# Optimization experiments

Measured on AMD Instinct MI355X. Metric: run time of the kernel, lower is better.

The kernel has to match this reference:

```python
import jax, jax.numpy as jnp
import numpy as np

B, N, D, H = 4, 4096, 256, 8
HD = D // H
EPS = 1e-09


def _feature_map(t):
    # ELU(x) + 1, strictly positive feature map (Katharopoulos et al. 2020)
    return jax.nn.elu(t) + 1.0


def setup_inputs() -> dict:
    key = jax.random.key(0)
    ks = jax.random.split(key, 8)
    s = 0.02  # weight init scale for numerical stability
    return {
        "x": jax.random.normal(ks[0], (B, N, D), dtype=jnp.float32),
        "prior": jax.random.normal(ks[1], (B, N, N), dtype=jnp.float32),
        "Wq": jax.random.normal(ks[2], (D, D), dtype=jnp.float32) * s,
        "Wk": jax.random.normal(ks[3], (D, D), dtype=jnp.float32) * s,
        "Wv": jax.random.normal(ks[4], (D, D), dtype=jnp.float32) * s,
        "bv": jax.random.normal(ks[5], (D,), dtype=jnp.float32) * s,
        "Wo": jax.random.normal(ks[6], (D, D), dtype=jnp.float32) * s,
        "bo": jax.random.normal(ks[7], (D,), dtype=jnp.float32) * s,
    }


def reference(x, prior, Wq, Wk, Wv, bv, Wo, bo):
    b, n, d = x.shape
    # bias: mean over last axis of prior -> (b, n, 1, 1), broadcast over heads/dims
    bias = jnp.mean(prior, axis=-1)[:, :, None, None]
    q = _feature_map(jnp.einsum("bnd,ed->bne", x, Wq).reshape(b, n, H, HD) + bias)
    padding_mask = jnp.all(q == 0, axis=-1)  # (b, n, H)
    k = _feature_map(jnp.einsum("bnd,ed->bne", x, Wk).reshape(b, n, H, HD))
    v = _feature_map((jnp.einsum("bnd,ed->bne", x, Wv) + bv).reshape(b, n, H, HD))
    # KV summary state: (b, h, m, d) with m = value dim, d = key feature dim
    kv = jnp.einsum("bnhd,bnhm->bhmd", k, v)
    # normalizer: q . sum_n(k)
    z = 1.0 / (jnp.einsum("bnhd,bhd->bnh", q, jnp.sum(k, axis=1)) + EPS)
    attn = jnp.einsum("bnhd,bhmd,bnh->bnhm", q, kv, z)
    attn = jnp.where(padding_mask[..., None], 0.0, attn)
    attn = attn.reshape(b, n, H * HD)
    return jnp.einsum("bnd,ed->bne", attn, Wo) + bo
```

## Files before the change

### kernel.cpp

```cpp
#include <hip/hip_runtime.h>
#include <hip/hip_bf16.h>
#include <math.h>

#define B_ 4
#define N_ 4096
#define D_ 256
#define H_ 8
#define HD_ 32
#define TOKENS (B_ * N_)
#define EPSF 1e-9f

typedef __bf16 bf16x8 __attribute__((ext_vector_type(8)));
typedef float f32x4 __attribute__((ext_vector_type(4)));
typedef ushort ushort8_t __attribute__((ext_vector_type(8)));

__device__ __forceinline__ float elu1(float x) { return x > 0.f ? x + 1.f : __expf(x); }

__device__ __forceinline__ ushort f2bf(float f) {
    __hip_bfloat16 h = __float2bfloat16(f);
    return *reinterpret_cast<ushort*>(&h);
}

#define GLOAD_LDS16(g, l)                                                              \
    __builtin_amdgcn_global_load_lds((__attribute__((address_space(1))) const void*)(g), \
                                     (__attribute__((address_space(3))) void*)(l), 16, 0, 0)

#define MFMA16(a, b, c) __builtin_amdgcn_mfma_f32_16x16x32_bf16((a), (b), (c), 0, 0, 0)

__global__ __launch_bounds__(256) void k_cvt_w(const float* __restrict__ Wq,
                                               const float* __restrict__ Wk,
                                               const float* __restrict__ Wv,
                                               const float* __restrict__ Wo,
                                               ushort* __restrict__ dst) {
    const int i = blockIdx.x * 256 + threadIdx.x;
    const int sel = i >> 13;
    const float* src = sel == 0 ? Wq : sel == 1 ? Wk : sel == 2 ? Wv : Wo;
    const int j = i & 8191;
    const float4* s = (const float4*)src + (size_t)j * 2;
    const float4 a = s[0], b = s[1];
    ushort8_t o;
    o[0] = f2bf(a.x); o[1] = f2bf(a.y); o[2] = f2bf(a.z); o[3] = f2bf(a.w);
    o[4] = f2bf(b.x); o[5] = f2bf(b.y); o[6] = f2bf(b.z); o[7] = f2bf(b.w);
    *((ushort8_t*)dst + i) = o;
}

__global__ __launch_bounds__(512, 2) void k_mix2(const float* __restrict__ prior,
                                                 const float* __restrict__ x,
                                                 const ushort* __restrict__ wq,
                                                 const ushort* __restrict__ wk,
                                                 const ushort* __restrict__ wv,
                                                 const float* __restrict__ bv,
                                                 float* __restrict__ bias_g,
                                                 ushort* __restrict__ qpre,
                                                 float* __restrict__ part) {
    __shared__ ushort As[32 * 256];
    __shared__ ushort Ws[3 * 256 * 32];
    const int t = threadIdx.x;
    const int w = t >> 6, lane = t & 63;
    const int bid = blockIdx.x;

    if (bid % 5 != 0) {
        const int bidx = bid - bid / 5 - 1;
        const int row = bidx * 8 + w;
        const f32x4* p = (const f32x4*)(prior + (size_t)row * N_);
        float s0 = 0.f, s1 = 0.f, s2 = 0.f, s3 = 0.f;
#pragma unroll
        for (int i = 0; i < 4; ++i) {
            const f32x4 a = __builtin_nontemporal_load(p + (i * 4 + 0) * 64 + lane);
            const f32x4 b = __builtin_nontemporal_load(p + (i * 4 + 1) * 64 + lane);
            const f32x4 c = __builtin_nontemporal_load(p + (i * 4 + 2) * 64 + lane);
            const f32x4 d = __builtin_nontemporal_load(p + (i * 4 + 3) * 64 + lane);
            s0 += a[0] + a[1] + a[2] + a[3];
            s1 += b[0] + b[1] + b[2] + b[3];
            s2 += c[0] + c[1] + c[2] + c[3];
            s3 += d[0] + d[1] + d[2] + d[3];
        }
        float s = (s0 + s1) + (s2 + s3);
#pragma unroll
        for (int off = 32; off; off >>= 1) s += __shfl_xor(s, off, 64);
        if (lane == 0) bias_g[row] = s * (1.0f / N_);
        return;
    }

    const int qidx = bid / 5;
    const int rowBase = qidx * 32;

    {
        const int r = t >> 4;
        const int c0 = (t & 15) * 4;
#pragma unroll
        for (int j = 0; j < 4; ++j) {
            const int c = c0 + j * 64;
            const float4 xv = *(const float4*)(x + (size_t)(rowBase + r) * 256 + c);
            ushort4 o;
            o.x = f2bf(xv.x); o.y = f2bf(xv.y); o.z = f2bf(xv.z); o.w = f2bf(xv.w);
            const int byte = (r * 512 + c * 2) ^ ((r & 7) << 4);
            *(ushort4*)((char*)As + byte) = o;
        }
    }

    const int wr = w >> 2, wc = w & 3;
    const int q_ = lane >> 4;
    f32x4 accq[4] = {}, acck[4] = {}, accv[4] = {};

    for (int kt = 0; kt < 256; kt += 32) {
        __syncthreads();
#pragma unroll
        for (int j = 0; j < 6; ++j) {
            const int c = j * 512 + t;
            const int idx = c & 1023;
            const int e = idx >> 2;
            const int pslot = idx & 3;
            const int qsrc = pslot ^ ((e >> 1) & 3);
            const ushort* srcm = (j < 2) ? wq : (j < 4) ? wk : wv;
            GLOAD_LDS16(srcm + (size_t)e * 256 + kt + qsrc * 8, (char*)Ws + c * 16);
        }
        __syncthreads();
        const int r = wr * 16 + (lane & 15);
        const int abyte = (r * 512 + (kt + q_ * 8) * 2) ^ ((r & 7) << 4);
        const bf16x8 af = *(const bf16x8*)((const char*)As + abyte);
#pragma unroll
        for (int n = 0; n < 4; ++n) {
            const int e = wc * 64 + n * 16 + (lane & 15);
            const int wbyte = e * 64 + ((q_ ^ ((e >> 1) & 3)) * 16);
            const bf16x8 bq = *(const bf16x8*)((const char*)Ws + wbyte);
            const bf16x8 bk = *(const bf16x8*)((const char*)Ws + 16384 + wbyte);
            const bf16x8 bw = *(const bf16x8*)((const char*)Ws + 32768 + wbyte);
            accq[n] = MFMA16(af, bq, accq[n]);
            acck[n] = MFMA16(af, bk, acck[n]);
            accv[n] = MFMA16(af, bw, accv[n]);
        }
    }

    __syncthreads();

    ushort* VT = Ws;
    ushort* KT = Ws + 8192;
#pragma unroll
    for (int n = 0; n < 4; ++n)
#pragma unroll
        for (int j = 0; j < 4; ++j) {
            const int rl = wr * 16 + (lane >> 4) * 4 + j;
            const int col = wc * 64 + n * 16 + (lane & 15);
            const size_t go = (size_t)(rowBase + rl) * 256 + col;
            qpre[go] = f2bf(accq[n][j]);
            const int head = col >> 5, dm = col & 31;
            KT[head * 1024 + dm * 32 + rl] = f2bf(elu1(acck[n][j]));
            VT[head * 1024 + dm * 32 + rl] = f2bf(elu1(accv[n][j] + bv[col]));
        }
    __syncthreads();

    const ushort* vtw = VT + w * 1024;
    const ushort* ktw = KT + w * 1024;
    bf16x8 av[2], bk2[2];
#pragma unroll
    for (int i = 0; i < 2; ++i) {
        av[i]  = *(const bf16x8*)(vtw + (i * 16 + (lane & 15)) * 32 + (lane >> 4) * 8);
        bk2[i] = *(const bf16x8*)(ktw + (i * 16 + (lane & 15)) * 32 + (lane >> 4) * 8);
    }
    bf16x8 ones;
#pragma unroll
    for (int i = 0; i < 8; ++i) ones[i] = (__bf16)1.0f;
    f32x4 kvacc[2][2] = {};
    f32x4 ks[2] = {};
#pragma unroll
    for (int mi = 0; mi < 2; ++mi)
#pragma unroll
        for (int di = 0; di < 2; ++di)
            kvacc[mi][di] = MFMA16(av[mi], bk2[di], kvacc[mi][di]);
#pragma unroll
    for (int di = 0; di < 2; ++di) ks[di] = MFMA16(ones, bk2[di], ks[di]);

    float* pp = part + (size_t)qidx * 8448 + w * 1056;
#pragma unroll
    for (int mi = 0; mi < 2; ++mi)
#pragma unroll
        for (int di = 0; di < 2; ++di)
#pragma unroll
            for (int j = 0; j < 4; ++j) {
                const int m = mi * 16 + (lane >> 4) * 4 + j;
                const int d = di * 16 + (lane & 15);
                pp[m * 32 + d] = kvacc[mi][di][j];
            }
    if ((lane >> 4) == 0) {
        pp[1024 + (lane & 15)] = ks[0][0];
        pp[1024 + 16 + (lane & 15)] = ks[1][0];
    }
}

__global__ __launch_bounds__(256) void k_kvred(const float* __restrict__ part,
                                               ushort* __restrict__ kvbf,
                                               float* __restrict__ ksum) {
    const int i = blockIdx.x * 256 + threadIdx.x;
    if (i >= 32 * 1056) return;
    const int bh = i / 1056, r = i - bh * 1056;
    const int b = bh >> 3, h = bh & 7;
    float s = 0.f;
#pragma unroll 8
    for (int c = 0; c < 128; ++c)
        s += part[(size_t)(b * 128 + c) * 8448 + h * 1056 + r];
    if (r < 1024) kvbf[(size_t)bh * 1024 + r] = f2bf(s);
    else          ksum[(size_t)bh * 32 + (r - 1024)] = s;
}

__global__ __launch_bounds__(512, 2) void k_fusedB(const ushort* __restrict__ qpre,
                                                   const float* __restrict__ bias_g,
                                                   const ushort* __restrict__ kvbf,
                                                   const float* __restrict__ ksum,
                                                   const ushort* __restrict__ wo,
                                                   const float* __restrict__ bo,
                                                   float* __restrict__ out) {
    __shared__ ushort qs[64 * 256];
    __shared__ ushort at_s[64 * 256];
    __shared__ ushort Ws2[256 * 32];
    __shared__ float den_s[64][8];
    const int t = threadIdx.x;
    const int w = t >> 6, lane = t & 63;
    const int tokBase = blockIdx.x * 64;
    const int b = tokBase >> 12;

#pragma unroll
    for (int j = 0; j < 4; ++j) {
        const int chunk = j * 512 + t;
        GLOAD_LDS16(qpre + (size_t)tokBase * 256 + (size_t)chunk * 8,
                    (char*)qs + chunk * 16);
    }
    __syncthreads();

    {
        const int r = t >> 3;
        const float brow = bias_g[tokBase + r];
        const int cb = (t & 7) * 32;
#pragma unroll
        for (int i = 0; i < 4; ++i) {
            bf16x8 qv = *(bf16x8*)(qs + r * 256 + cb + i * 8);
#pragma unroll
            for (int j = 0; j < 8; ++j) qv[j] = (__bf16)elu1((float)qv[j] + brow);
            *(bf16x8*)(qs + r * 256 + cb + i * 8) = qv;
        }
    }
    __syncthreads();

    {
        const int tok = t >> 3, h = t & 7;
        const float* ksp = ksum + (size_t)(b * H_ + h) * HD_;
        float den = 0.f;
#pragma unroll
        for (int i = 0; i < 4; ++i) {
            const bf16x8 qv = *(const bf16x8*)(qs + tok * 256 + h * HD_ + i * 8);
            const f32x4 k0 = *(const f32x4*)(ksp + i * 8);
            const f32x4 k1 = *(const f32x4*)(ksp + i * 8 + 4);
#pragma unroll
            for (int j = 0; j < 4; ++j) {
                den = fmaf((float)qv[j], k0[j], den);
                den = fmaf((float)qv[j + 4], k1[j], den);
            }
        }
        den_s[tok][h] = den + EPSF;
    }

    bf16x8 af[4], bfk[2];
#pragma unroll
    for (int mi = 0; mi < 4; ++mi)
        af[mi] = *(const bf16x8*)(qs + (mi * 16 + (lane & 15)) * 256 + w * HD_ +
                                  (lane >> 4) * 8);
#pragma unroll
    for (int ni = 0; ni < 2; ++ni)
        bfk[ni] = *(const bf16x8*)(kvbf +
                                   ((size_t)(b * H_ + w) * HD_ + ni * 16 + (lane & 15)) * HD_ +
                                   (lane >> 4) * 8);
    f32x4 nacc[4][2] = {};
#pragma unroll
    for (int mi = 0; mi < 4; ++mi)
#pragma unroll
        for (int ni = 0; ni < 2; ++ni)
            nacc[mi][ni] = MFMA16(af[mi], bfk[ni], nacc[mi][ni]);

    __syncthreads();

#pragma unroll
    for (int mi = 0; mi < 4; ++mi)
#pragma unroll
        for (int ni = 0; ni < 2; ++ni)
#pragma unroll
            for (int j = 0; j < 4; ++j) {
                const int tok = mi * 16 + (lane >> 4) * 4 + j;
                const int c2 = w * HD_ + ni * 16 + (lane & 15);
                const float a = nacc[mi][ni][j] / den_s[tok][w];
                const int byte = (tok * 512 + c2 * 2) ^ ((tok & 7) << 4);
                *(ushort*)((char*)at_s + byte) = f2bf(a);
            }

    const int wr = w >> 2, wc = w & 3;
    const int q_ = lane >> 4;
    f32x4 acc[2][4] = {};
    for (int kt = 0; kt < 256; kt += 32) {
        __syncthreads();
#pragma unroll
        for (int j = 0; j < 2; ++j) {
            const int ch = j * 512 + t;
            const int e = ch >> 2;
            const int pslot = ch & 3;
            const int qsrc = pslot ^ ((e >> 1) & 3);
            GLOAD_LDS16(wo + (size_t)e * 256 + kt + qsrc * 8, (char*)Ws2 + ch * 16);
        }
        __syncthreads();
        bf16x8 af2[2];
#pragma unroll
        for (int mm = 0; mm < 2; ++mm) {
            const int r = wr * 32 + mm * 16 + (lane & 15);
            const int byte = (r * 512 + (kt + q_ * 8) * 2) ^ ((r & 7) << 4);
            af2[mm] = *(const bf16x8*)((const char*)at_s + byte);
        }
#pragma unroll
        for (int n = 0; n < 4; ++n) {
            const int e = wc * 64 + n * 16 + (lane & 15);
            const int wbyte = e * 64 + ((q_ ^ ((e >> 1) & 3)) * 16);
            const bf16x8 bw = *(const bf16x8*)((const char*)Ws2 + wbyte);
#pragma unroll
            for (int mm = 0; mm < 2; ++mm)
                acc[mm][n] = MFMA16(af2[mm], bw, acc[mm][n]);
        }
    }
#pragma unroll
    for (int mm = 0; mm < 2; ++mm)
#pragma unroll
        for (int n = 0; n < 4; ++n)
#pragma unroll
            for (int j = 0; j < 4; ++j) {
                const int row = tokBase + wr * 32 + mm * 16 + (lane >> 4) * 4 + j;
                const int col = wc * 64 + n * 16 + (lane & 15);
                out[(size_t)row * 256 + col] = acc[mm][n][j] + bo[col];
            }
}

extern "C" void kernel_launch(void* const* d_in, const int* in_sizes, int n_in,
                              void* d_out, int out_size, void* d_ws, size_t ws_size,
                              hipStream_t stream) {
    const float* x     = (const float*)d_in[0];
    const float* prior = (const float*)d_in[1];
    const float* Wq    = (const float*)d_in[2];
    const float* Wk    = (const float*)d_in[3];
    const float* Wv    = (const float*)d_in[4];
    const float* bv    = (const float*)d_in[5];
    const float* Wo    = (const float*)d_in[6];
    const float* bo    = (const float*)d_in[7];
    float* out = (float*)d_out;

    char* w8 = (char*)d_ws;
    ushort* qpre = (ushort*)w8;
    ushort* wqb  = qpre + (size_t)TOKENS * D_;
    ushort* wkb  = wqb + 65536;
    ushort* wvb  = wkb + 65536;
    ushort* wob  = wvb + 65536;
    ushort* kvbf = wob + 65536;
    float* ksb   = (float*)(kvbf + 32768);
    float* bias  = ksb + 1024;
    float* part  = bias + TOKENS;

    k_cvt_w<<<128, 256, 0, stream>>>(Wq, Wk, Wv, Wo, wqb);

    k_mix2<<<2560, 512, 0, stream>>>(prior, x, wqb, wkb, wvb, bv, bias, qpre, part);

    k_kvred<<<132, 256, 0, stream>>>(part, kvbf, ksb);

    k_fusedB<<<256, 512, 0, stream>>>(qpre, bias, kvbf, ksb, wob, bo, out);
}
```

Measured before the change: 90.19 us.

## Interleave prior row-mean streaming into the QKV projection GEMM loop

Removes the separate bias-reduction blocks and has each GEMM block stream its own 32 prior rows (4 per wave), software-pipelined across the 8 k-tile iterations so the loads overlap the MFMA work. The grid shrinks from 2560 to 512 blocks, and launch bounds rise to 4 blocks per CU so enough waves stay resident to cover memory latency. The risk is higher register pressure from the 8 in-flight f32x4 prefetch buffers under the tighter occupancy target, and a less balanced bandwidth-bound phase.

```diff
diff --git a/kernel.cpp b/kernel.cpp
--- a/kernel.cpp
+++ b/kernel.cpp
@@ -44,7 +44,7 @@
     *((ushort8_t*)dst + i) = o;
 }
 
-__global__ __launch_bounds__(512, 2) void k_mix2(const float* __restrict__ prior,
+__global__ __launch_bounds__(512, 4) void k_mix8(const float* __restrict__ prior,
                                                  const float* __restrict__ x,
                                                  const ushort* __restrict__ wq,
                                                  const ushort* __restrict__ wk,
@@ -57,32 +57,7 @@
     __shared__ ushort Ws[3 * 256 * 32];
     const int t = threadIdx.x;
     const int w = t >> 6, lane = t & 63;
-    const int bid = blockIdx.x;
-
-    if (bid % 5 != 0) {
-        const int bidx = bid - bid / 5 - 1;
-        const int row = bidx * 8 + w;
-        const f32x4* p = (const f32x4*)(prior + (size_t)row * N_);
-        float s0 = 0.f, s1 = 0.f, s2 = 0.f, s3 = 0.f;
-#pragma unroll
-        for (int i = 0; i < 4; ++i) {
-            const f32x4 a = __builtin_nontemporal_load(p + (i * 4 + 0) * 64 + lane);
-            const f32x4 b = __builtin_nontemporal_load(p + (i * 4 + 1) * 64 + lane);
-            const f32x4 c = __builtin_nontemporal_load(p + (i * 4 + 2) * 64 + lane);
-            const f32x4 d = __builtin_nontemporal_load(p + (i * 4 + 3) * 64 + lane);
-            s0 += a[0] + a[1] + a[2] + a[3];
-            s1 += b[0] + b[1] + b[2] + b[3];
-            s2 += c[0] + c[1] + c[2] + c[3];
-            s3 += d[0] + d[1] + d[2] + d[3];
-        }
-        float s = (s0 + s1) + (s2 + s3);
-#pragma unroll
-        for (int off = 32; off; off >>= 1) s += __shfl_xor(s, off, 64);
-        if (lane == 0) bias_g[row] = s * (1.0f / N_);
-        return;
-    }
-
-    const int qidx = bid / 5;
+    const int qidx = blockIdx.x;
     const int rowBase = qidx * 32;
 
     {
@@ -99,11 +74,49 @@
         }
     }
 
+    const int brow0 = rowBase + w * 4;
+    const f32x4* bp = (const f32x4*)(prior + (size_t)brow0 * N_);
+    float s0 = 0.f, s1 = 0.f, s2 = 0.f, s3 = 0.f;
+    f32x4 bb0, bb1, bb2, bb3, bb4, bb5, bb6, bb7;
+
+#define BIAS_ISSUE(IT)                                                          \
+    {                                                                           \
+        const f32x4* rp_ = bp + ((IT) >> 1) * 1024 + ((IT) & 1) * 512 + lane;   \
+        bb0 = __builtin_nontemporal_load(rp_ + 0 * 64);                         \
+        bb1 = __builtin_nontemporal_load(rp_ + 1 * 64);                         \
+        bb2 = __builtin_nontemporal_load(rp_ + 2 * 64);                         \
+        bb3 = __builtin_nontemporal_load(rp_ + 3 * 64);                         \
+        bb4 = __builtin_nontemporal_load(rp_ + 4 * 64);                         \
+        bb5 = __builtin_nontemporal_load(rp_ + 5 * 64);                         \
+        bb6 = __builtin_nontemporal_load(rp_ + 6 * 64);                         \
+        bb7 = __builtin_nontemporal_load(rp_ + 7 * 64);                         \
+    }
+#define BIAS_CONSUME(IT)                                                        \
+    {                                                                           \
+        float ps_ = (bb0[0] + bb0[1] + bb0[2] + bb0[3]) +                       \
+                    (bb1[0] + bb1[1] + bb1[2] + bb1[3]) +                       \
+                    (bb2[0] + bb2[1] + bb2[2] + bb2[3]) +                       \
+                    (bb3[0] + bb3[1] + bb3[2] + bb3[3]) +                       \
+                    (bb4[0] + bb4[1] + bb4[2] + bb4[3]) +                       \
+                    (bb5[0] + bb5[1] + bb5[2] + bb5[3]) +                       \
+                    (bb6[0] + bb6[1] + bb6[2] + bb6[3]) +                       \
+                    (bb7[0] + bb7[1] + bb7[2] + bb7[3]);                        \
+        const int br_ = (IT) >> 1;                                              \
+        if (br_ == 0) s0 += ps_;                                                \
+        else if (br_ == 1) s1 += ps_;                                           \
+        else if (br_ == 2) s2 += ps_;                                           \
+        else s3 += ps_;                                                         \
+    }
+
+    BIAS_ISSUE(0)
+
     const int wr = w >> 2, wc = w & 3;
     const int q_ = lane >> 4;
     f32x4 accq[4] = {}, acck[4] = {}, accv[4] = {};
 
-    for (int kt = 0; kt < 256; kt += 32) {
+#pragma unroll
+    for (int it = 0; it < 8; ++it) {
+        const int kt = it * 32;
         __syncthreads();
 #pragma unroll
         for (int j = 0; j < 6; ++j) {
@@ -115,6 +128,8 @@
             const ushort* srcm = (j < 2) ? wq : (j < 4) ? wk : wv;
             GLOAD_LDS16(srcm + (size_t)e * 256 + kt + qsrc * 8, (char*)Ws + c * 16);
         }
+        BIAS_CONSUME(it)
+        if (it < 7) BIAS_ISSUE(it + 1)
         __syncthreads();
         const int r = wr * 16 + (lane & 15);
         const int abyte = (r * 512 + (kt + q_ * 8) * 2) ^ ((r & 7) << 4);
@@ -131,6 +146,17 @@
             accv[n] = MFMA16(af, bw, accv[n]);
         }
     }
+#undef BIAS_ISSUE
+#undef BIAS_CONSUME
+
+#define BIAS_RED(sv, rr)                                                    \
+    {                                                                       \
+        float v_ = sv;                                                      \
+        for (int off = 32; off; off >>= 1) v_ += __shfl_xor(v_, off, 64);   \
+        if (lane == 0) bias_g[brow0 + rr] = v_ * (1.0f / N_);               \
+    }
+    BIAS_RED(s0, 0) BIAS_RED(s1, 1) BIAS_RED(s2, 2) BIAS_RED(s3, 3)
+#undef BIAS_RED
 
     __syncthreads();
 
@@ -360,7 +386,7 @@
 
     k_cvt_w<<<128, 256, 0, stream>>>(Wq, Wk, Wv, Wo, wqb);
 
-    k_mix2<<<2560, 512, 0, stream>>>(prior, x, wqb, wkb, wvb, bv, bias, qpre, part);
+    k_mix8<<<512, 512, 0, stream>>>(prior, x, wqb, wkb, wvb, bv, bias, qpre, part);
 
     k_kvred<<<132, 256, 0, stream>>>(part, kvbf, ksb);
 
```

Result: slower. 162.0 us (+79.6%).
